# Optimization experiments

Measured on AMD Instinct MI355X. Metric: run time of the kernel, lower is better.

The kernel has to match this reference:

```python
import jax, jax.numpy as jnp
import numpy as np

N, E, C, NA, NR, H = 50000, 320000, 64, 10, 8, 64
AVG_NUM_NEIGHBORS = 16.0
WEIGHT_NUMEL = 5 * C  # 5 uvu tensor-product paths, one weight per channel


def setup_inputs() -> dict:
    key = jax.random.key(0)
    ks = jax.random.split(key, 18)
    rn = lambda k, s: jax.random.normal(k, s, dtype=jnp.float32)
    return {
        "node_attrs": jax.random.uniform(ks[0], (N, NA), dtype=jnp.float32),
        "node_feats_s": rn(ks[1], (N, C)),
        "node_feats_v": rn(ks[2], (N, C, 3)),
        "edge_sh0": jnp.ones((E, 1), jnp.float32),          # Y_00 (constant)
        "edge_sh1": rn(ks[3], (E, 3)),                       # Y_1m
        "edge_feats": rn(ks[4], (E, NR)),                    # radial scalars (0e)
        "senders": jax.random.randint(ks[5], (E,), 0, N, dtype=jnp.int32),
        "receivers": jax.random.randint(ks[6], (E,), 0, N, dtype=jnp.int32),
        # skip-connection tensor-product linear: (C*NA)x0e -> Cx0e, (C*NA)x1o -> Cx1o
        "W_sc_s": rn(ks[7], (C * NA, C)),
        "W_sc_v": rn(ks[8], (C * NA, C)),
        # self linear on node_feats (per-irrep channel mixing)
        "W_self_s": rn(ks[9], (C, C)),
        "W_self_v": rn(ks[10], (C, C)),
        # radial MLP: NR -> 64 -> 64 -> 64 -> weight_numel
        "W1": rn(ks[11], (NR, H)),
        "W2": rn(ks[12], (H, H)),
        "W3": rn(ks[13], (H, H)),
        "W4": rn(ks[14], (H, WEIGHT_NUMEL)),
        # output linear: mid irreps 2Cx0e + 3Cx1o -> target Cx0e + Cx1o
        "W_out_s": rn(ks[15], (2 * C, C)),
        "W_out_v": rn(ks[16], (3 * C, C)),
    }


def reference(node_attrs, node_feats_s, node_feats_v, edge_sh0, edge_sh1,
              edge_feats, senders, receivers, W_sc_s, W_sc_v, W_self_s,
              W_self_v, W1, W2, W3, W4, W_out_s, W_out_v):
    n, c = node_feats_s.shape
    na = node_attrs.shape[1]
    # ---- skip connection: Linear(hidden)(node_feats (x) node_attrs) ----
    ts = (node_feats_s[:, :, None] * node_attrs[:, None, :]).reshape(n, c * na)
    tv = (node_feats_v[:, :, None, :] * node_attrs[:, None, :, None]).reshape(n, c * na, 3)
    inv_sc = 1.0 / np.sqrt(c * na)
    sc_s = (ts @ W_sc_s) * inv_sc
    sc_v = jnp.einsum('nkx,kd->ndx', tv, W_sc_v) * inv_sc
    # ---- self linear on node_feats ----
    inv_c = 1.0 / np.sqrt(c)
    s = (node_feats_s @ W_self_s) * inv_c
    v = jnp.einsum('ncx,cd->ndx', node_feats_v, W_self_v) * inv_c
    # ---- radial MLP -> per-edge tensor-product weights ----
    h = jax.nn.silu((edge_feats @ W1) / np.sqrt(edge_feats.shape[1]))
    h = jax.nn.silu((h @ W2) / np.sqrt(H))
    h = jax.nn.silu((h @ W3) / np.sqrt(H))
    w = (h @ W4) / np.sqrt(H)                      # [E, 5C]
    w1, w2, w3, w4, w5 = jnp.split(w, 5, axis=1)   # one weight per path per channel
    # ---- gather -> per-edge equivariant tensor product -> scatter-add ----
    se = s[senders]                                # [E, C]
    ve = v[senders]                                # [E, C, 3]
    p1 = w1 * se * edge_sh0                                              # 0e x 0e -> 0e
    p2 = w2 * jnp.einsum('ecx,ex->ec', ve, edge_sh1) / np.sqrt(3.0)      # 1o x 1o -> 0e
    p3 = (w3 * se)[:, :, None] * edge_sh1[:, None, :]                    # 0e x 1o -> 1o
    p4 = (w4 * edge_sh0)[:, :, None] * ve                                # 1o x 0e -> 1o
    p5 = w5[:, :, None] * jnp.cross(ve, edge_sh1[:, None, :]) / np.sqrt(2.0)  # 1o x 1o -> 1o
    mji_s = jnp.concatenate([p1, p2], axis=1)      # [E, 2C]
    mji_v = jnp.concatenate([p3, p4, p5], axis=1)  # [E, 3C, 3]
    m_s = jnp.zeros((n, 2 * c), mji_s.dtype).at[receivers].add(mji_s)
    m_v = jnp.zeros((n, 3 * c, 3), mji_v.dtype).at[receivers].add(mji_v)
    # ---- output linear / avg_num_neighbors ----
    out_s = (m_s @ W_out_s) / (np.sqrt(2 * c) * AVG_NUM_NEIGHBORS)
    out_v = jnp.einsum('nkx,kd->ndx', m_v, W_out_v) / (np.sqrt(3 * c) * AVG_NUM_NEIGHBORS)
    return (out_s, out_v, sc_s, sc_v)
```

## Files before the change

kernel.cpp:

```cpp
#include <hip/hip_runtime.h>

#define NC    64
#define NATTR 10
#define NH    64
#define NRAD  8
#define TEB   128
#define MPN   704

__device__ __forceinline__ float silu_f(float x) { return x / (1.0f + __expf(-x)); }

typedef __fp16 h2v __attribute__((ext_vector_type(2)));

__device__ __forceinline__ unsigned int pkh(float lo, float hi)
{
    union { h2v h; unsigned int u; } cv;
    cv.h = __builtin_amdgcn_cvt_pkrtz(lo, hi);
    return cv.u;
}
__device__ __forceinline__ h2v uph(unsigned int u)
{
    union { unsigned int u; h2v h; } cv;
    cv.u = u;
    return cv.h;
}

#if defined(__has_builtin)
#if __has_builtin(__builtin_amdgcn_fdot2)
#define HAS_FDOT2 1
#endif
#endif

__device__ __forceinline__ float fd2(unsigned int a, unsigned int b, float c)
{
#ifdef HAS_FDOT2
    return __builtin_amdgcn_fdot2(uph(a), uph(b), c, false);
#else
    h2v x = uph(a), y = uph(b);
    return c + (float)x[0] * (float)y[0] + (float)x[1] * (float)y[1];
#endif
}


__global__ void hist_kernel(const int* __restrict__ rcv, int* __restrict__ deg, int E)
{
    int e = blockIdx.x * 256 + threadIdx.x;
    if (e < E) atomicAdd(&deg[rcv[e]], 1);
}

__global__ __launch_bounds__(256)
void scan_kernel(const int* __restrict__ deg, int* __restrict__ row_ptr, int N)
{
    __shared__ int sums[256];
    __shared__ int offs[257];
    const int t = threadIdx.x;
    const int chunk = (N + 255) / 256;
    int b = t * chunk, e = min(N, b + chunk);
    int s = 0;
    for (int k = b; k < e; k++) s += deg[k];
    sums[t] = s;
    __syncthreads();
    if (t == 0) {
        int run = 0;
        for (int i = 0; i < 256; i++) { offs[i] = run; run += sums[i]; }
        offs[256] = run;
    }
    __syncthreads();
    int run = offs[t];
    for (int k = b; k < e; k++) { row_ptr[k] = run; run += deg[k]; }
    if (t == 255) row_ptr[N] = offs[256];
}

__global__ void fill_kernel(const int* __restrict__ rcv, const int* __restrict__ row_ptr,
                            int* __restrict__ cursor, int* __restrict__ eidx, int E)
{
    int e = blockIdx.x * 256 + threadIdx.x;
    if (e < E) {
        int r = rcv[e];
        int pos = atomicAdd(&cursor[r], 1);
        eidx[row_ptr[r] + pos] = e;
    }
}

__global__ __launch_bounds__(256)
void self_kernel(const float* __restrict__ fs, const float* __restrict__ fv,
                 const float* __restrict__ Wes, const float* __restrict__ Wev,
                 float* __restrict__ out, int N)
{
    __shared__ float s_l[4][NC];
    __shared__ float v_l[4][3][NC];
    const int t = threadIdx.x, wv = t >> 6, lane = t & 63;
    const int n = blockIdx.x * 4 + wv;

    if (n < N) {
        s_l[wv][lane] = fs[(size_t)n * NC + lane];
        v_l[wv][0][lane] = fv[(size_t)n * NC * 3 + lane * 3 + 0];
        v_l[wv][1][lane] = fv[(size_t)n * NC * 3 + lane * 3 + 1];
        v_l[wv][2][lane] = fv[(size_t)n * NC * 3 + lane * 3 + 2];
    }
    __syncthreads();
    if (n >= N) return;

    const int d = lane;
    float a = 0.f, bx = 0.f, by = 0.f, bz = 0.f;
    #pragma unroll 8
    for (int c = 0; c < NC; c++) {
        float ws = Wes[c * NC + d];
        float wvv = Wev[c * NC + d];
        a  += s_l[wv][c] * ws;
        bx += v_l[wv][0][c] * wvv;
        by += v_l[wv][1][c] * wvv;
        bz += v_l[wv][2][c] * wvv;
    }
    out[(size_t)N * 256 + (size_t)n * NC + d]            = a  * 0.125f;
    out[(size_t)N * 320 + (size_t)n * 192 +       d]     = bx * 0.125f;
    out[(size_t)N * 320 + (size_t)n * 192 +  64 + d]     = by * 0.125f;
    out[(size_t)N * 320 + (size_t)n * 192 + 128 + d]     = bz * 0.125f;
}

__global__ __launch_bounds__(128, 3)
void edge_kernel(const float* __restrict__ ef, const float* __restrict__ sh0,
                 const float* __restrict__ sh1,
                 const int* __restrict__ snd, const int* __restrict__ rcv,
                 const float* __restrict__ W1, const float* __restrict__ W2,
                 const float* __restrict__ W3, const float* __restrict__ W4,
                 const float* __restrict__ s_st, const float* __restrict__ v_st,
                 const int* __restrict__ eidx,
                 float* __restrict__ m, int E)
{
    __shared__ unsigned int h_l[TEB][36];
    __shared__ float sh1_l[TEB][3];
    __shared__ float sh0_l[TEB];
    __shared__ int   snd_l[TEB];
    __shared__ int   rcv_l[TEB];

    const int t = threadIdx.x;
    const int p0 = blockIdx.x * TEB;

    {
        int p = p0 + t;
        bool valid = p < E;
        int e = valid ? eidx[p] : 0;
        snd_l[t] = valid ? snd[e] : 0;
        rcv_l[t] = valid ? rcv[e] : -1;
        sh0_l[t] = valid ? sh0[e] : 0.f;
        sh1_l[t][0] = valid ? sh1[(size_t)e * 3 + 0] : 0.f;
        sh1_l[t][1] = valid ? sh1[(size_t)e * 3 + 1] : 0.f;
        sh1_l[t][2] = valid ? sh1[(size_t)e * 3 + 2] : 0.f;

        float x[NRAD];
        #pragma unroll
        for (int r = 0; r < NRAD; r++)
            x[r] = valid ? ef[(size_t)e * NRAD + r] : 0.f;

        float h1[NH];
        #pragma unroll
        for (int j = 0; j < NH; j++) {
            float a = 0.f;
            #pragma unroll
            for (int r = 0; r < NRAD; r++) a += x[r] * W1[r * NH + j];
            h1[j] = silu_f(a * 0.35355339059327373f);
        }

        unsigned int h2p[32];
        for (int jt = 0; jt < 16; jt++) {
            float a0 = 0.f, a1 = 0.f, a2 = 0.f, a3 = 0.f;
            #pragma unroll
            for (int c = 0; c < NH; c++) {
                float hv = h1[c];
                const float* wr = W2 + c * NH + jt * 4;
                a0 += hv * wr[0]; a1 += hv * wr[1];
                a2 += hv * wr[2]; a3 += hv * wr[3];
            }
            h2p[jt * 2 + 0] = pkh(silu_f(a0 * 0.125f), silu_f(a1 * 0.125f));
            h2p[jt * 2 + 1] = pkh(silu_f(a2 * 0.125f), silu_f(a3 * 0.125f));
        }
        for (int jt = 0; jt < 16; jt++) {
            float a0 = 0.f, a1 = 0.f, a2 = 0.f, a3 = 0.f;
            #pragma unroll
            for (int cp = 0; cp < 32; cp++) {
                h2v u = uph(h2p[cp]);
                float hl = (float)u[0], hh = (float)u[1];
                const float* wr0 = W3 + (2 * cp) * NH + jt * 4;
                const float* wr1 = W3 + (2 * cp + 1) * NH + jt * 4;
                a0 += hl * wr0[0] + hh * wr1[0];
                a1 += hl * wr0[1] + hh * wr1[1];
                a2 += hl * wr0[2] + hh * wr1[2];
                a3 += hl * wr0[3] + hh * wr1[3];
            }
            h_l[t][jt * 2 + 0] = pkh(silu_f(a0 * 0.125f), silu_f(a1 * 0.125f));
            h_l[t][jt * 2 + 1] = pkh(silu_f(a2 * 0.125f), silu_f(a3 * 0.125f));
        }
    }
    __syncthreads();

    const int wv = t >> 6, lane = t & 63;
    const int base = wv * 64;
    const int v_sd = snd_l[base + lane];
    const int v_rc = rcv_l[base + lane];

#define DOT32(W, res)                                                     \
    {                                                                     \
        const uint4* hp_ = (const uint4*)(&h_l[pos][0]);                  \
        float w_ = 0.f;                                                   \
        _Pragma("unroll")                                                 \
        for (int q8 = 0; q8 < 8; q8++) {                                  \
            uint4 hu = hp_[q8];                                           \
            w_ = fd2(hu.x, W[q8 * 4 + 0], w_);                            \
            w_ = fd2(hu.y, W[q8 * 4 + 1], w_);                            \
            w_ = fd2(hu.z, W[q8 * 4 + 2], w_);                            \
            w_ = fd2(hu.w, W[q8 * 4 + 3], w_);                            \
        }                                                                 \
        res = w_ * 0.125f;                                \
    }

    {
        unsigned int W0[32];
        #pragma unroll
        for (int q = 0; q < 32; q++)
            W0[q] = pkh(W4[(2 * q) * 320 + lane], W4[(2 * q + 1) * 320 + lane]);
        float gc = s_st[(size_t)__builtin_amdgcn_readlane(v_sd, 0) * NC + lane];
        float gn = s_st[(size_t)__builtin_amdgcn_readlane(v_sd, 1) * NC + lane];
        int r_cur = -1;
        float acc = 0.f;
        #pragma unroll 2
        for (int ei = 0; ei < 64; ei++) {
            const int pn = (ei + 2 > 63) ? 63 : ei + 2;
            const float gf = s_st[(size_t)__builtin_amdgcn_readlane(v_sd, pn) * NC + lane];
            const int r = __builtin_amdgcn_readlane(v_rc, ei);
            if (r != r_cur) {
                if (r_cur >= 0) {
                    unsafeAtomicAdd(m + (size_t)r_cur * MPN + lane, acc);
                    acc = 0.f;
                }
                r_cur = r;
            }
            if (r >= 0) {
                const int pos = base + ei;
                float w;
                DOT32(W0, w);
                acc += w * gc * sh0_l[pos];
            }
            gc = gn; gn = gf;
        }
        if (r_cur >= 0) unsafeAtomicAdd(m + (size_t)r_cur * MPN + lane, acc);
    }

    {
        unsigned int W0[32];
        #pragma unroll
        for (int q = 0; q < 32; q++)
            W0[q] = pkh(W4[(2 * q) * 320 + 128 + lane], W4[(2 * q + 1) * 320 + 128 + lane]);
        float gc = s_st[(size_t)__builtin_amdgcn_readlane(v_sd, 0) * NC + lane];
        float gn = s_st[(size_t)__builtin_amdgcn_readlane(v_sd, 1) * NC + lane];
        int r_cur = -1;
        float ax = 0.f, ay = 0.f, az = 0.f;
        #pragma unroll 2
        for (int ei = 0; ei < 64; ei++) {
            const int pn = (ei + 2 > 63) ? 63 : ei + 2;
            const float gf = s_st[(size_t)__builtin_amdgcn_readlane(v_sd, pn) * NC + lane];
            const int r = __builtin_amdgcn_readlane(v_rc, ei);
            if (r != r_cur) {
                if (r_cur >= 0) {
                    float* mb = m + (size_t)r_cur * MPN + 128;
                    unsafeAtomicAdd(mb + lane,       ax);
                    unsafeAtomicAdd(mb + 192 + lane, ay);
                    unsafeAtomicAdd(mb + 384 + lane, az);
                    ax = ay = az = 0.f;
                }
                r_cur = r;
            }
            if (r >= 0) {
                const int pos = base + ei;
                float w;
                DOT32(W0, w);
                float t3 = w * gc;
                ax += t3 * sh1_l[pos][0];
                ay += t3 * sh1_l[pos][1];
                az += t3 * sh1_l[pos][2];
            }
            gc = gn; gn = gf;
        }
        if (r_cur >= 0) {
            float* mb = m + (size_t)r_cur * MPN + 128;
            unsafeAtomicAdd(mb + lane,       ax);
            unsafeAtomicAdd(mb + 192 + lane, ay);
            unsafeAtomicAdd(mb + 384 + lane, az);
        }
    }

    {
        unsigned int W0[32];
        #pragma unroll
        for (int q = 0; q < 32; q++)
            W0[q] = pkh(W4[(2 * q) * 320 + 64 + lane], W4[(2 * q + 1) * 320 + 64 + lane]);
        float gxc, gyc, gzc, gxn, gyn, gzn;
        {
            size_t sb0 = (size_t)__builtin_amdgcn_readlane(v_sd, 0) * 192;
            size_t sb1 = (size_t)__builtin_amdgcn_readlane(v_sd, 1) * 192;
            gxc = v_st[sb0 + lane]; gyc = v_st[sb0 + 64 + lane]; gzc = v_st[sb0 + 128 + lane];
            gxn = v_st[sb1 + lane]; gyn = v_st[sb1 + 64 + lane]; gzn = v_st[sb1 + 128 + lane];
        }
        int r_cur = -1;
        float acc = 0.f;
        #pragma unroll 2
        for (int ei = 0; ei < 64; ei++) {
            const int pn = (ei + 2 > 63) ? 63 : ei + 2;
            size_t sb = (size_t)__builtin_amdgcn_readlane(v_sd, pn) * 192;
            const float gxf = v_st[sb + lane];
            const float gyf = v_st[sb + 64 + lane];
            const float gzf = v_st[sb + 128 + lane];
            const int r = __builtin_amdgcn_readlane(v_rc, ei);
            if (r != r_cur) {
                if (r_cur >= 0) {
                    unsafeAtomicAdd(m + (size_t)r_cur * MPN + 64 + lane, acc);
                    acc = 0.f;
                }
                r_cur = r;
            }
            if (r >= 0) {
                const int pos = base + ei;
                float w;
                DOT32(W0, w);
                float dot = gxc * sh1_l[pos][0] + gyc * sh1_l[pos][1] + gzc * sh1_l[pos][2];
                acc += w * dot * 0.5773502691896258f;
            }
            gxc = gxn; gyc = gyn; gzc = gzn;
            gxn = gxf; gyn = gyf; gzn = gzf;
        }
        if (r_cur >= 0) unsafeAtomicAdd(m + (size_t)r_cur * MPN + 64 + lane, acc);
    }

    {
        unsigned int W0[32];
        #pragma unroll
        for (int q = 0; q < 32; q++)
            W0[q] = pkh(W4[(2 * q) * 320 + 192 + lane], W4[(2 * q + 1) * 320 + 192 + lane]);
        float gxc, gyc, gzc, gxn, gyn, gzn;
        {
            size_t sb0 = (size_t)__builtin_amdgcn_readlane(v_sd, 0) * 192;
            size_t sb1 = (size_t)__builtin_amdgcn_readlane(v_sd, 1) * 192;
            gxc = v_st[sb0 + lane]; gyc = v_st[sb0 + 64 + lane]; gzc = v_st[sb0 + 128 + lane];
            gxn = v_st[sb1 + lane]; gyn = v_st[sb1 + 64 + lane]; gzn = v_st[sb1 + 128 + lane];
        }
        int r_cur = -1;
        float ax = 0.f, ay = 0.f, az = 0.f;
        #pragma unroll 2
        for (int ei = 0; ei < 64; ei++) {
            const int pn = (ei + 2 > 63) ? 63 : ei + 2;
            size_t sb = (size_t)__builtin_amdgcn_readlane(v_sd, pn) * 192;
            const float gxf = v_st[sb + lane];
            const float gyf = v_st[sb + 64 + lane];
            const float gzf = v_st[sb + 128 + lane];
            const int r = __builtin_amdgcn_readlane(v_rc, ei);
            if (r != r_cur) {
                if (r_cur >= 0) {
                    float* mb = m + (size_t)r_cur * MPN + 128 + 64;
                    unsafeAtomicAdd(mb + lane,       ax);
                    unsafeAtomicAdd(mb + 192 + lane, ay);
                    unsafeAtomicAdd(mb + 384 + lane, az);
                    ax = ay = az = 0.f;
                }
                r_cur = r;
            }
            if (r >= 0) {
                const int pos = base + ei;
                float w;
                DOT32(W0, w);
                float w4s = w * sh0_l[pos];
                ax += w4s * gxc; ay += w4s * gyc; az += w4s * gzc;
            }
            gxc = gxn; gyc = gyn; gzc = gzn;
            gxn = gxf; gyn = gyf; gzn = gzf;
        }
        if (r_cur >= 0) {
            float* mb = m + (size_t)r_cur * MPN + 128 + 64;
            unsafeAtomicAdd(mb + lane,       ax);
            unsafeAtomicAdd(mb + 192 + lane, ay);
            unsafeAtomicAdd(mb + 384 + lane, az);
        }
    }

    {
        unsigned int W0[32];
        #pragma unroll
        for (int q = 0; q < 32; q++)
            W0[q] = pkh(W4[(2 * q) * 320 + 256 + lane], W4[(2 * q + 1) * 320 + 256 + lane]);
        float gxc, gyc, gzc, gxn, gyn, gzn;
        {
            size_t sb0 = (size_t)__builtin_amdgcn_readlane(v_sd, 0) * 192;
            size_t sb1 = (size_t)__builtin_amdgcn_readlane(v_sd, 1) * 192;
            gxc = v_st[sb0 + lane]; gyc = v_st[sb0 + 64 + lane]; gzc = v_st[sb0 + 128 + lane];
            gxn = v_st[sb1 + lane]; gyn = v_st[sb1 + 64 + lane]; gzn = v_st[sb1 + 128 + lane];
        }
        int r_cur = -1;
        float ax = 0.f, ay = 0.f, az = 0.f;
        #pragma unroll 2
        for (int ei = 0; ei < 64; ei++) {
            const int pn = (ei + 2 > 63) ? 63 : ei + 2;
            size_t sb = (size_t)__builtin_amdgcn_readlane(v_sd, pn) * 192;
            const float gxf = v_st[sb + lane];
            const float gyf = v_st[sb + 64 + lane];
            const float gzf = v_st[sb + 128 + lane];
            const int r = __builtin_amdgcn_readlane(v_rc, ei);
            if (r != r_cur) {
                if (r_cur >= 0) {
                    float* mb = m + (size_t)r_cur * MPN + 128 + 128;
                    unsafeAtomicAdd(mb + lane,       ax);
                    unsafeAtomicAdd(mb + 192 + lane, ay);
                    unsafeAtomicAdd(mb + 384 + lane, az);
                    ax = ay = az = 0.f;
                }
                r_cur = r;
            }
            if (r >= 0) {
                const int pos = base + ei;
                float w;
                DOT32(W0, w);
                float shx = sh1_l[pos][0], shy = sh1_l[pos][1], shz = sh1_l[pos][2];
                float w5s = w * 0.7071067811865476f;
                ax += w5s * (gyc * shz - gzc * shy);
                ay += w5s * (gzc * shx - gxc * shz);
                az += w5s * (gxc * shy - gyc * shx);
            }
            gxc = gxn; gyc = gyn; gzc = gzn;
            gxn = gxf; gyn = gyf; gzn = gzf;
        }
        if (r_cur >= 0) {
            float* mb = m + (size_t)r_cur * MPN + 128 + 128;
            unsafeAtomicAdd(mb + lane,       ax);
            unsafeAtomicAdd(mb + 192 + lane, ay);
            unsafeAtomicAdd(mb + 384 + lane, az);
        }
    }
#undef DOT32
}

__global__ __launch_bounds__(256)
void sc_kernel(const float* __restrict__ attrs, const float* __restrict__ fs,
               const float* __restrict__ fv,
               const float* __restrict__ Wss, const float* __restrict__ Wsv,
               float* __restrict__ out, int N)
{
    __shared__ unsigned int At[32][68];
    __shared__ unsigned int Bt[32][68];

    const int part = blockIdx.y;
    const int n0 = blockIdx.x * 64;
    const int t = threadIdx.x;
    const int tn = t & 15, td = t >> 4;
    const float* W = (part == 0) ? Wss : Wsv;
    const int x = part - 1;

    float acc[4][4];
    #pragma unroll
    for (int i = 0; i < 4; i++)
        #pragma unroll
        for (int j = 0; j < 4; j++) acc[i][j] = 0.f;

    for (int kt = 0; kt < 10; kt++) {
        __syncthreads();
        for (int i = t; i < 2048; i += 256) {
            int n = i >> 5, kp = i & 31;
            int k0 = kt * 64 + kp * 2;
            int c0 = k0 / 10, a0 = k0 - c0 * 10;
            int k1 = k0 + 1;
            int c1 = k1 / 10, a1 = k1 - c1 * 10;
            int ng = n0 + n;
            float f0 = 0.f, f1 = 0.f;
            if (ng < N) {
                float fa = (part == 0) ? fs[(size_t)ng * 64 + c0]
                                       : fv[((size_t)ng * 64 + c0) * 3 + x];
                float fb = (part == 0) ? fs[(size_t)ng * 64 + c1]
                                       : fv[((size_t)ng * 64 + c1) * 3 + x];
                f0 = fa * attrs[(size_t)ng * 10 + a0];
                f1 = fb * attrs[(size_t)ng * 10 + a1];
            }
            At[kp][n] = pkh(f0, f1);
        }
        for (int i = t; i < 2048; i += 256) {
            int kp = i >> 6, d = i & 63;
            Bt[kp][d] = pkh(W[(size_t)(kt * 64 + 2 * kp) * 64 + d],
                            W[(size_t)(kt * 64 + 2 * kp + 1) * 64 + d]);
        }
        __syncthreads();
        #pragma unroll 8
        for (int kp = 0; kp < 32; kp++) {
            uint4 au = *(const uint4*)(&At[kp][tn * 4]);
            uint4 bu = *(const uint4*)(&Bt[kp][td * 4]);
            unsigned int aa[4] = {au.x, au.y, au.z, au.w};
            unsigned int bb[4] = {bu.x, bu.y, bu.z, bu.w};
            #pragma unroll
            for (int i = 0; i < 4; i++)
                #pragma unroll
                for (int j = 0; j < 4; j++)
                    acc[i][j] = fd2(aa[i], bb[j], acc[i][j]);
        }
    }

    const float inv_sc = 0.03952847075210474f;
    #pragma unroll
    for (int i = 0; i < 4; i++) {
        int ng = n0 + tn * 4 + i;
        if (ng >= N) continue;
        #pragma unroll
        for (int j = 0; j < 4; j++) {
            int d = td * 4 + j;
            float v = acc[i][j] * inv_sc;
            if (part == 0) out[(size_t)N * 256 + (size_t)ng * 64 + d] = v;
            else           out[(size_t)N * 320 + (size_t)ng * 192 + d * 3 + x] = v;
        }
    }
}

__global__ __launch_bounds__(256)
void outlin_kernel(const float* __restrict__ m,
                   const float* __restrict__ Wos, const float* __restrict__ Wov,
                   float* __restrict__ out, int N)
{
    __shared__ unsigned int At[32][68];
    __shared__ unsigned int Bt[32][68];

    const int part = blockIdx.y;
    const int n0 = blockIdx.x * 64;
    const int t = threadIdx.x;
    const int tn = t & 15, td = t >> 4;
    const int x = part - 1;
    const int ntiles = (part == 0) ? 2 : 3;
    const int aoff = (part == 0) ? 0 : 128 + x * 192;
    const float* W = (part == 0) ? Wos : Wov;

    float acc[4][4];
    #pragma unroll
    for (int i = 0; i < 4; i++)
        #pragma unroll
        for (int j = 0; j < 4; j++) acc[i][j] = 0.f;

    for (int kt = 0; kt < ntiles; kt++) {
        __syncthreads();
        for (int i = t; i < 2048; i += 256) {
            int n = i >> 5, kp = i & 31;
            int ng = n0 + n;
            float f0 = 0.f, f1 = 0.f;
            if (ng < N) {
                const float* mp = m + (size_t)ng * MPN + aoff + kt * 64 + kp * 2;
                f0 = mp[0]; f1 = mp[1];
            }
            At[kp][n] = pkh(f0, f1);
        }
        for (int i = t; i < 2048; i += 256) {
            int kp = i >> 6, d = i & 63;
            Bt[kp][d] = pkh(W[(size_t)(kt * 64 + 2 * kp) * 64 + d],
                            W[(size_t)(kt * 64 + 2 * kp + 1) * 64 + d]);
        }
        __syncthreads();
        #pragma unroll 8
        for (int kp = 0; kp < 32; kp++) {
            uint4 au = *(const uint4*)(&At[kp][tn * 4]);
            uint4 bu = *(const uint4*)(&Bt[kp][td * 4]);
            unsigned int aa[4] = {au.x, au.y, au.z, au.w};
            unsigned int bb[4] = {bu.x, bu.y, bu.z, bu.w};
            #pragma unroll
            for (int i = 0; i < 4; i++)
                #pragma unroll
                for (int j = 0; j < 4; j++)
                    acc[i][j] = fd2(aa[i], bb[j], acc[i][j]);
        }
    }

    const float scale = (part == 0) ? 0.005524271728019903f
                                    : 0.004510527174164819f;
    #pragma unroll
    for (int i = 0; i < 4; i++) {
        int ng = n0 + tn * 4 + i;
        if (ng >= N) continue;
        #pragma unroll
        for (int j = 0; j < 4; j++) {
            int d = td * 4 + j;
            float v = acc[i][j] * scale;
            if (part == 0) out[(size_t)ng * 64 + d] = v;
            else           out[(size_t)N * 64 + (size_t)ng * 192 + d * 3 + x] = v;
        }
    }
}

extern "C" void kernel_launch(void* const* d_in, const int* in_sizes, int n_in,
                              void* d_out, int out_size, void* d_ws, size_t ws_size,
                              hipStream_t stream)
{
    const float* attrs = (const float*)d_in[0];
    const float* fs    = (const float*)d_in[1];
    const float* fv    = (const float*)d_in[2];
    const float* sh0   = (const float*)d_in[3];
    const float* sh1   = (const float*)d_in[4];
    const float* ef    = (const float*)d_in[5];
    const int*   snd   = (const int*)d_in[6];
    const int*   rcv   = (const int*)d_in[7];
    const float* Wss   = (const float*)d_in[8];
    const float* Wsv   = (const float*)d_in[9];
    const float* Wes   = (const float*)d_in[10];
    const float* Wev   = (const float*)d_in[11];
    const float* W1    = (const float*)d_in[12];
    const float* W2    = (const float*)d_in[13];
    const float* W3    = (const float*)d_in[14];
    const float* W4    = (const float*)d_in[15];
    const float* Wos   = (const float*)d_in[16];
    const float* Wov   = (const float*)d_in[17];

    const int N = in_sizes[0] / NATTR;
    const int E = in_sizes[6];

    float* out = (float*)d_out;
    const float* s_st = out + (size_t)N * 256;
    const float* v_st = out + (size_t)N * 320;

    int* deg     = (int*)d_out;
    int* cursor  = deg + N;
    int* row_ptr = cursor + N;
    int* eidx    = row_ptr + N + 1;

    float* m = (float*)d_ws;

    (void)hipMemsetAsync(deg, 0, (size_t)2 * N * sizeof(int), stream);
    (void)hipMemsetAsync(m, 0, (size_t)N * MPN * sizeof(float), stream);

    const int eb = (E + 255) / 256;
    hist_kernel<<<eb, 256, 0, stream>>>(rcv, deg, E);
    scan_kernel<<<1, 256, 0, stream>>>(deg, row_ptr, N);
    fill_kernel<<<eb, 256, 0, stream>>>(rcv, row_ptr, cursor, eidx, E);

    self_kernel<<<(N + 3) / 4, 256, 0, stream>>>(fs, fv, Wes, Wev, out, N);

    const int nbe = (E + TEB - 1) / TEB;
    edge_kernel<<<nbe, 128, 0, stream>>>(ef, sh0, sh1, snd, rcv,
                                         W1, W2, W3, W4, s_st, v_st,
                                         eidx, m, E);

    dim3 g_out((N + 63) / 64, 4);
    outlin_kernel<<<g_out, 256, 0, stream>>>(m, Wos, Wov, out, N);

    dim3 g_sc((N + 63) / 64, 4);
    sc_kernel<<<g_sc, 256, 0, stream>>>(attrs, fs, fv, Wss, Wsv, out, N);
}
```

Baseline: 1.213 ms.

## Fuse five per-path edge loops into two passes sharing gathers and hidden loads

Replaces five separate per-path passes over each wave's 64 edges with two fused passes: one for the scalar-sender paths (p1, p3) and one for the vector-sender paths (p2, p4, p5). Each pass evaluates two or three radial-weight dot products per hidden-vector load from LDS and gathers sender features once instead of once per path. The gather prefetch distance grows from 2 to 4 and the unroll factor from 2 to 4. In exchange it keeps 64 to 96 packed weight registers live, plus more accumulators and prefetch registers, which raises register pressure and may reduce occupancy.

```diff
diff --git a/kernel.cpp b/kernel.cpp
--- a/kernel.cpp
+++ b/kernel.cpp
@@ -38,6 +38,44 @@
     h2v x = uph(a), y = uph(b);
     return c + (float)x[0] * (float)y[0] + (float)x[1] * (float)y[1];
 #endif
+}
+
+__device__ __forceinline__ void dot2w(const uint4* hp,
+    const unsigned int (&Wa)[32], const unsigned int (&Wb)[32],
+    float& ra, float& rb)
+{
+    float a = 0.f, b = 0.f;
+    #pragma unroll
+    for (int q8 = 0; q8 < 8; q8++) {
+        uint4 hu = hp[q8];
+        unsigned int hw[4] = {hu.x, hu.y, hu.z, hu.w};
+        #pragma unroll
+        for (int k = 0; k < 4; k++) {
+            a = fd2(hw[k], Wa[q8 * 4 + k], a);
+            b = fd2(hw[k], Wb[q8 * 4 + k], b);
+        }
+    }
+    ra = a * 0.125f; rb = b * 0.125f;
+}
+
+__device__ __forceinline__ void dot3w(const uint4* hp,
+    const unsigned int (&Wa)[32], const unsigned int (&Wb)[32],
+    const unsigned int (&Wc)[32],
+    float& ra, float& rb, float& rc)
+{
+    float a = 0.f, b = 0.f, c = 0.f;
+    #pragma unroll
+    for (int q8 = 0; q8 < 8; q8++) {
+        uint4 hu = hp[q8];
+        unsigned int hw[4] = {hu.x, hu.y, hu.z, hu.w};
+        #pragma unroll
+        for (int k = 0; k < 4; k++) {
+            a = fd2(hw[k], Wa[q8 * 4 + k], a);
+            b = fd2(hw[k], Wb[q8 * 4 + k], b);
+            c = fd2(hw[k], Wc[q8 * 4 + k], c);
+        }
+    }
+    ra = a * 0.125f; rb = b * 0.125f; rc = c * 0.125f;
 }
 
 
@@ -198,113 +236,94 @@
     const int v_sd = snd_l[base + lane];
     const int v_rc = rcv_l[base + lane];
 
-#define DOT32(W, res)                                                     \
-    {                                                                     \
-        const uint4* hp_ = (const uint4*)(&h_l[pos][0]);                  \
-        float w_ = 0.f;                                                   \
-        _Pragma("unroll")                                                 \
-        for (int q8 = 0; q8 < 8; q8++) {                                  \
-            uint4 hu = hp_[q8];                                           \
-            w_ = fd2(hu.x, W[q8 * 4 + 0], w_);                            \
-            w_ = fd2(hu.y, W[q8 * 4 + 1], w_);                            \
-            w_ = fd2(hu.z, W[q8 * 4 + 2], w_);                            \
-            w_ = fd2(hu.w, W[q8 * 4 + 3], w_);                            \
-        }                                                                 \
-        res = w_ * 0.125f;                                \
-    }
-
     {
-        unsigned int W0[32];
-        #pragma unroll
-        for (int q = 0; q < 32; q++)
-            W0[q] = pkh(W4[(2 * q) * 320 + lane], W4[(2 * q + 1) * 320 + lane]);
-        float gc = s_st[(size_t)__builtin_amdgcn_readlane(v_sd, 0) * NC + lane];
-        float gn = s_st[(size_t)__builtin_amdgcn_readlane(v_sd, 1) * NC + lane];
+        unsigned int WA[32], WC[32];
+        #pragma unroll
+        for (int q = 0; q < 32; q++) {
+            WA[q] = pkh(W4[(2 * q) * 320 + lane],       W4[(2 * q + 1) * 320 + lane]);
+            WC[q] = pkh(W4[(2 * q) * 320 + 128 + lane], W4[(2 * q + 1) * 320 + 128 + lane]);
+        }
+        #pragma unroll
+        for (int q = 0; q < 32; q++) {
+            asm volatile("" : "+v"(WA[q]));
+            asm volatile("" : "+v"(WC[q]));
+        }
+        float g0 = s_st[(size_t)__builtin_amdgcn_readlane(v_sd, 0) * NC + lane];
+        float g1 = s_st[(size_t)__builtin_amdgcn_readlane(v_sd, 1) * NC + lane];
+        float g2 = s_st[(size_t)__builtin_amdgcn_readlane(v_sd, 2) * NC + lane];
+        float g3 = s_st[(size_t)__builtin_amdgcn_readlane(v_sd, 3) * NC + lane];
         int r_cur = -1;
-        float acc = 0.f;
-        #pragma unroll 2
+        float a1 = 0.f, a3x = 0.f, a3y = 0.f, a3z = 0.f;
+        #pragma unroll 4
         for (int ei = 0; ei < 64; ei++) {
-            const int pn = (ei + 2 > 63) ? 63 : ei + 2;
+            const int pn = (ei + 4 > 63) ? 63 : ei + 4;
             const float gf = s_st[(size_t)__builtin_amdgcn_readlane(v_sd, pn) * NC + lane];
             const int r = __builtin_amdgcn_readlane(v_rc, ei);
             if (r != r_cur) {
                 if (r_cur >= 0) {
-                    unsafeAtomicAdd(m + (size_t)r_cur * MPN + lane, acc);
-                    acc = 0.f;
+                    float* mb = m + (size_t)r_cur * MPN;
+                    unsafeAtomicAdd(mb + lane,             a1);
+                    unsafeAtomicAdd(mb + 128 + lane,       a3x);
+                    unsafeAtomicAdd(mb + 128 + 192 + lane, a3y);
+                    unsafeAtomicAdd(mb + 128 + 384 + lane, a3z);
+                    a1 = a3x = a3y = a3z = 0.f;
                 }
                 r_cur = r;
             }
             if (r >= 0) {
                 const int pos = base + ei;
-                float w;
-                DOT32(W0, w);
-                acc += w * gc * sh0_l[pos];
-            }
-            gc = gn; gn = gf;
-        }
-        if (r_cur >= 0) unsafeAtomicAdd(m + (size_t)r_cur * MPN + lane, acc);
+                float w1w, w3w;
+                dot2w((const uint4*)(&h_l[pos][0]), WA, WC, w1w, w3w);
+                float se = g0;
+                a1 += w1w * se * sh0_l[pos];
+                float t3 = w3w * se;
+                a3x += t3 * sh1_l[pos][0];
+                a3y += t3 * sh1_l[pos][1];
+                a3z += t3 * sh1_l[pos][2];
+            }
+            g0 = g1; g1 = g2; g2 = g3; g3 = gf;
+        }
+        if (r_cur >= 0) {
+            float* mb = m + (size_t)r_cur * MPN;
+            unsafeAtomicAdd(mb + lane,             a1);
+            unsafeAtomicAdd(mb + 128 + lane,       a3x);
+            unsafeAtomicAdd(mb + 128 + 192 + lane, a3y);
+            unsafeAtomicAdd(mb + 128 + 384 + lane, a3z);
+        }
     }
 
     {
-        unsigned int W0[32];
-        #pragma unroll
-        for (int q = 0; q < 32; q++)
-            W0[q] = pkh(W4[(2 * q) * 320 + 128 + lane], W4[(2 * q + 1) * 320 + 128 + lane]);
-        float gc = s_st[(size_t)__builtin_amdgcn_readlane(v_sd, 0) * NC + lane];
-        float gn = s_st[(size_t)__builtin_amdgcn_readlane(v_sd, 1) * NC + lane];
+        unsigned int WB[32], WD[32], WE[32];
+        #pragma unroll
+        for (int q = 0; q < 32; q++) {
+            WB[q] = pkh(W4[(2 * q) * 320 +  64 + lane], W4[(2 * q + 1) * 320 +  64 + lane]);
+            WD[q] = pkh(W4[(2 * q) * 320 + 192 + lane], W4[(2 * q + 1) * 320 + 192 + lane]);
+            WE[q] = pkh(W4[(2 * q) * 320 + 256 + lane], W4[(2 * q + 1) * 320 + 256 + lane]);
+        }
+        #pragma unroll
+        for (int q = 0; q < 32; q++) {
+            asm volatile("" : "+v"(WB[q]));
+            asm volatile("" : "+v"(WD[q]));
+            asm volatile("" : "+v"(WE[q]));
+        }
+        float gx0, gy0, gz0, gx1, gy1, gz1, gx2, gy2, gz2, gx3, gy3, gz3;
+        {
+            size_t s0 = (size_t)__builtin_amdgcn_readlane(v_sd, 0) * 192;
+            size_t s1 = (size_t)__builtin_amdgcn_readlane(v_sd, 1) * 192;
+            size_t s2 = (size_t)__builtin_amdgcn_readlane(v_sd, 2) * 192;
+            size_t s3 = (size_t)__builtin_amdgcn_readlane(v_sd, 3) * 192;
+            gx0 = v_st[s0 + lane]; gy0 = v_st[s0 + 64 + lane]; gz0 = v_st[s0 + 128 + lane];
+            gx1 = v_st[s1 + lane]; gy1 = v_st[s1 + 64 + lane]; gz1 = v_st[s1 + 128 + lane];
+            gx2 = v_st[s2 + lane]; gy2 = v_st[s2 + 64 + lane]; gz2 = v_st[s2 + 128 + lane];
+            gx3 = v_st[s3 + lane]; gy3 = v_st[s3 + 64 + lane]; gz3 = v_st[s3 + 128 + lane];
+        }
         int r_cur = -1;
-        float ax = 0.f, ay = 0.f, az = 0.f;
-        #pragma unroll 2
+        float a2 = 0.f;
+        float a4x = 0.f, a4y = 0.f, a4z = 0.f;
+        float a5x = 0.f, a5y = 0.f, a5z = 0.f;
+        #pragma unroll 4
         for (int ei = 0; ei < 64; ei++) {
-            const int pn = (ei + 2 > 63) ? 63 : ei + 2;
-            const float gf = s_st[(size_t)__builtin_amdgcn_readlane(v_sd, pn) * NC + lane];
-            const int r = __builtin_amdgcn_readlane(v_rc, ei);
-            if (r != r_cur) {
-                if (r_cur >= 0) {
-                    float* mb = m + (size_t)r_cur * MPN + 128;
-                    unsafeAtomicAdd(mb + lane,       ax);
-                    unsafeAtomicAdd(mb + 192 + lane, ay);
-                    unsafeAtomicAdd(mb + 384 + lane, az);
-                    ax = ay = az = 0.f;
-                }
-                r_cur = r;
-            }
-            if (r >= 0) {
-                const int pos = base + ei;
-                float w;
-                DOT32(W0, w);
-                float t3 = w * gc;
-                ax += t3 * sh1_l[pos][0];
-                ay += t3 * sh1_l[pos][1];
-                az += t3 * sh1_l[pos][2];
-            }
-            gc = gn; gn = gf;
-        }
-        if (r_cur >= 0) {
-            float* mb = m + (size_t)r_cur * MPN + 128;
-            unsafeAtomicAdd(mb + lane,       ax);
-            unsafeAtomicAdd(mb + 192 + lane, ay);
-            unsafeAtomicAdd(mb + 384 + lane, az);
-        }
-    }
-
-    {
-        unsigned int W0[32];
-        #pragma unroll
-        for (int q = 0; q < 32; q++)
-            W0[q] = pkh(W4[(2 * q) * 320 + 64 + lane], W4[(2 * q + 1) * 320 + 64 + lane]);
-        float gxc, gyc, gzc, gxn, gyn, gzn;
-        {
-            size_t sb0 = (size_t)__builtin_amdgcn_readlane(v_sd, 0) * 192;
-            size_t sb1 = (size_t)__builtin_amdgcn_readlane(v_sd, 1) * 192;
-            gxc = v_st[sb0 + lane]; gyc = v_st[sb0 + 64 + lane]; gzc = v_st[sb0 + 128 + lane];
-            gxn = v_st[sb1 + lane]; gyn = v_st[sb1 + 64 + lane]; gzn = v_st[sb1 + 128 + lane];
-        }
-        int r_cur = -1;
-        float acc = 0.f;
-        #pragma unroll 2
-        for (int ei = 0; ei < 64; ei++) {
-            const int pn = (ei + 2 > 63) ? 63 : ei + 2;
+            const int pn = (ei + 4 > 63) ? 63 : ei + 4;
             size_t sb = (size_t)__builtin_amdgcn_readlane(v_sd, pn) * 192;
             const float gxf = v_st[sb + lane];
             const float gyf = v_st[sb + 64 + lane];
@@ -312,127 +331,49 @@
             const int r = __builtin_amdgcn_readlane(v_rc, ei);
             if (r != r_cur) {
                 if (r_cur >= 0) {
-                    unsafeAtomicAdd(m + (size_t)r_cur * MPN + 64 + lane, acc);
-                    acc = 0.f;
+                    float* mb = m + (size_t)r_cur * MPN;
+                    unsafeAtomicAdd(mb + 64 + lane,              a2);
+                    unsafeAtomicAdd(mb + 128 + 64 + lane,        a4x);
+                    unsafeAtomicAdd(mb + 128 + 192 + 64 + lane,  a4y);
+                    unsafeAtomicAdd(mb + 128 + 384 + 64 + lane,  a4z);
+                    unsafeAtomicAdd(mb + 128 + 128 + lane,       a5x);
+                    unsafeAtomicAdd(mb + 128 + 192 + 128 + lane, a5y);
+                    unsafeAtomicAdd(mb + 128 + 384 + 128 + lane, a5z);
+                    a2 = a4x = a4y = a4z = a5x = a5y = a5z = 0.f;
                 }
                 r_cur = r;
             }
             if (r >= 0) {
                 const int pos = base + ei;
-                float w;
-                DOT32(W0, w);
-                float dot = gxc * sh1_l[pos][0] + gyc * sh1_l[pos][1] + gzc * sh1_l[pos][2];
-                acc += w * dot * 0.5773502691896258f;
-            }
-            gxc = gxn; gyc = gyn; gzc = gzn;
-            gxn = gxf; gyn = gyf; gzn = gzf;
-        }
-        if (r_cur >= 0) unsafeAtomicAdd(m + (size_t)r_cur * MPN + 64 + lane, acc);
-    }
-
-    {
-        unsigned int W0[32];
-        #pragma unroll
-        for (int q = 0; q < 32; q++)
-            W0[q] = pkh(W4[(2 * q) * 320 + 192 + lane], W4[(2 * q + 1) * 320 + 192 + lane]);
-        float gxc, gyc, gzc, gxn, gyn, gzn;
-        {
-            size_t sb0 = (size_t)__builtin_amdgcn_readlane(v_sd, 0) * 192;
-            size_t sb1 = (size_t)__builtin_amdgcn_readlane(v_sd, 1) * 192;
-            gxc = v_st[sb0 + lane]; gyc = v_st[sb0 + 64 + lane]; gzc = v_st[sb0 + 128 + lane];
-            gxn = v_st[sb1 + lane]; gyn = v_st[sb1 + 64 + lane]; gzn = v_st[sb1 + 128 + lane];
-        }
-        int r_cur = -1;
-        float ax = 0.f, ay = 0.f, az = 0.f;
-        #pragma unroll 2
-        for (int ei = 0; ei < 64; ei++) {
-            const int pn = (ei + 2 > 63) ? 63 : ei + 2;
-            size_t sb = (size_t)__builtin_amdgcn_readlane(v_sd, pn) * 192;
-            const float gxf = v_st[sb + lane];
-            const float gyf = v_st[sb + 64 + lane];
-            const float gzf = v_st[sb + 128 + lane];
-            const int r = __builtin_amdgcn_readlane(v_rc, ei);
-            if (r != r_cur) {
-                if (r_cur >= 0) {
-                    float* mb = m + (size_t)r_cur * MPN + 128 + 64;
-                    unsafeAtomicAdd(mb + lane,       ax);
-                    unsafeAtomicAdd(mb + 192 + lane, ay);
-                    unsafeAtomicAdd(mb + 384 + lane, az);
-                    ax = ay = az = 0.f;
-                }
-                r_cur = r;
-            }
-            if (r >= 0) {
-                const int pos = base + ei;
-                float w;
-                DOT32(W0, w);
-                float w4s = w * sh0_l[pos];
-                ax += w4s * gxc; ay += w4s * gyc; az += w4s * gzc;
-            }
-            gxc = gxn; gyc = gyn; gzc = gzn;
-            gxn = gxf; gyn = gyf; gzn = gzf;
+                float w2w, w4w, w5w;
+                dot3w((const uint4*)(&h_l[pos][0]), WB, WD, WE, w2w, w4w, w5w);
+                float vx = gx0, vy = gy0, vz = gz0;
+                float shx = sh1_l[pos][0], shy = sh1_l[pos][1], shz = sh1_l[pos][2];
+                float dot = vx * shx + vy * shy + vz * shz;
+                a2 += w2w * dot * 0.5773502691896258f;
+                float w4s = w4w * sh0_l[pos];
+                a4x += w4s * vx; a4y += w4s * vy; a4z += w4s * vz;
+                float w5s = w5w * 0.7071067811865476f;
+                a5x += w5s * (vy * shz - vz * shy);
+                a5y += w5s * (vz * shx - vx * shz);
+                a5z += w5s * (vx * shy - vy * shx);
+            }
+            gx0 = gx1; gy0 = gy1; gz0 = gz1;
+            gx1 = gx2; gy1 = gy2; gz1 = gz2;
+            gx2 = gx3; gy2 = gy3; gz2 = gz3;
+            gx3 = gxf; gy3 = gyf; gz3 = gzf;
         }
         if (r_cur >= 0) {
-            float* mb = m + (size_t)r_cur * MPN + 128 + 64;
-            unsafeAtomicAdd(mb + lane,       ax);
-            unsafeAtomicAdd(mb + 192 + lane, ay);
-            unsafeAtomicAdd(mb + 384 + lane, az);
-        }
-    }
-
-    {
-        unsigned int W0[32];
-        #pragma unroll
-        for (int q = 0; q < 32; q++)
-            W0[q] = pkh(W4[(2 * q) * 320 + 256 + lane], W4[(2 * q + 1) * 320 + 256 + lane]);
-        float gxc, gyc, gzc, gxn, gyn, gzn;
-        {
-            size_t sb0 = (size_t)__builtin_amdgcn_readlane(v_sd, 0) * 192;
-            size_t sb1 = (size_t)__builtin_amdgcn_readlane(v_sd, 1) * 192;
-            gxc = v_st[sb0 + lane]; gyc = v_st[sb0 + 64 + lane]; gzc = v_st[sb0 + 128 + lane];
-            gxn = v_st[sb1 + lane]; gyn = v_st[sb1 + 64 + lane]; gzn = v_st[sb1 + 128 + lane];
-        }
-        int r_cur = -1;
-        float ax = 0.f, ay = 0.f, az = 0.f;
-        #pragma unroll 2
-        for (int ei = 0; ei < 64; ei++) {
-            const int pn = (ei + 2 > 63) ? 63 : ei + 2;
-            size_t sb = (size_t)__builtin_amdgcn_readlane(v_sd, pn) * 192;
-            const float gxf = v_st[sb + lane];
-            const float gyf = v_st[sb + 64 + lane];
-            const float gzf = v_st[sb + 128 + lane];
-            const int r = __builtin_amdgcn_readlane(v_rc, ei);
-            if (r != r_cur) {
-                if (r_cur >= 0) {
-                    float* mb = m + (size_t)r_cur * MPN + 128 + 128;
-                    unsafeAtomicAdd(mb + lane,       ax);
-                    unsafeAtomicAdd(mb + 192 + lane, ay);
-                    unsafeAtomicAdd(mb + 384 + lane, az);
-                    ax = ay = az = 0.f;
-                }
-                r_cur = r;
-            }
-            if (r >= 0) {
-                const int pos = base + ei;
-                float w;
-                DOT32(W0, w);
-                float shx = sh1_l[pos][0], shy = sh1_l[pos][1], shz = sh1_l[pos][2];
-                float w5s = w * 0.7071067811865476f;
-                ax += w5s * (gyc * shz - gzc * shy);
-                ay += w5s * (gzc * shx - gxc * shz);
-                az += w5s * (gxc * shy - gyc * shx);
-            }
-            gxc = gxn; gyc = gyn; gzc = gzn;
-            gxn = gxf; gyn = gyf; gzn = gzf;
-        }
-        if (r_cur >= 0) {
-            float* mb = m + (size_t)r_cur * MPN + 128 + 128;
-            unsafeAtomicAdd(mb + lane,       ax);
-            unsafeAtomicAdd(mb + 192 + lane, ay);
-            unsafeAtomicAdd(mb + 384 + lane, az);
-        }
-    }
-#undef DOT32
+            float* mb = m + (size_t)r_cur * MPN;
+            unsafeAtomicAdd(mb + 64 + lane,              a2);
+            unsafeAtomicAdd(mb + 128 + 64 + lane,        a4x);
+            unsafeAtomicAdd(mb + 128 + 192 + 64 + lane,  a4y);
+            unsafeAtomicAdd(mb + 128 + 384 + 64 + lane,  a4z);
+            unsafeAtomicAdd(mb + 128 + 128 + lane,       a5x);
+            unsafeAtomicAdd(mb + 128 + 192 + 128 + lane, a5y);
+            unsafeAtomicAdd(mb + 128 + 384 + 128 + lane, a5z);
+        }
+    }
 }
 
 __global__ __launch_bounds__(256)
```

Result: faster. 1.073 ms (-11.5%).
